# Kernel tuning notes

Measured on AMD Instinct MI355X. Metric: run time of the kernel, lower is better.

The kernel has to match this reference:

```python
import jax, jax.numpy as jnp
import numpy as np

N = 100000      # nodes
E = 1600000     # edges (before self-loops)
F_IN = 16       # num_node_features
HID = 16        # hid
HEADS = 4       # in_head == out_head
B = 64          # num graphs
G = 16          # num_global_features
NEG_SLOPE = 0.2


def gat_conv(x, src, dst, W, a_src, a_dst, b, concat):
    """PyG-style GATConv. x:[N,F], W:[F,H*C], a_src/a_dst:[H,C], b:[H*C] or [C]."""
    n = x.shape[0]
    H, C = a_src.shape
    h = (x @ W).reshape(n, H, C)                       # [N,H,C]
    alpha_s = (h * a_src).sum(-1)                      # [N,H]
    alpha_d = (h * a_dst).sum(-1)                      # [N,H]
    e = jax.nn.leaky_relu(alpha_s[src] + alpha_d[dst], NEG_SLOPE)  # [E',H]
    # segment softmax over destination nodes (stable; max is grad-free)
    m = jax.lax.stop_gradient(jax.ops.segment_max(e, dst, num_segments=n))
    ex = jnp.exp(e - m[dst])
    denom = jax.ops.segment_sum(ex, dst, num_segments=n)
    alpha = ex / (denom[dst] + 1e-16)                  # [E',H]
    out = jax.ops.segment_sum(h[src] * alpha[:, :, None], dst, num_segments=n)  # [N,H,C]
    out = out.reshape(n, H * C) if concat else out.mean(axis=1)
    return out + b


def setup_inputs() -> dict:
    key = jax.random.key(0)
    ks = jax.random.split(key, 24)
    s = 0.1
    inp = {
        "x": jax.random.normal(ks[0], (N, F_IN), jnp.float32),
        "stats": jax.random.normal(ks[1], (B, G), jnp.float32),
        # conv1: F_IN -> HID, heads=HEADS, concat=True
        "W1": jax.random.normal(ks[2], (F_IN, HEADS * HID), jnp.float32) * s,
        "a1s": jax.random.normal(ks[3], (HEADS, HID), jnp.float32) * s,
        "a1d": jax.random.normal(ks[4], (HEADS, HID), jnp.float32) * s,
        "b1": jnp.zeros((HEADS * HID,), jnp.float32),
        # conv2: HID*HEADS -> HID, heads=HEADS, concat=False
        "W2": jax.random.normal(ks[5], (HEADS * HID, HEADS * HID), jnp.float32) * s,
        "a2s": jax.random.normal(ks[6], (HEADS, HID), jnp.float32) * s,
        "a2d": jax.random.normal(ks[7], (HEADS, HID), jnp.float32) * s,
        "b2": jnp.zeros((HID,), jnp.float32),
        # conv3: HID -> HID, heads=HEADS, concat=False
        "W3": jax.random.normal(ks[8], (HID, HEADS * HID), jnp.float32) * s,
        "a3s": jax.random.normal(ks[9], (HEADS, HID), jnp.float32) * s,
        "a3d": jax.random.normal(ks[10], (HEADS, HID), jnp.float32) * s,
        "b3": jnp.zeros((HID,), jnp.float32),
        # MLP head
        "fw1": jax.random.normal(ks[11], (HID + G, 32), jnp.float32) * s,
        "fb1": jnp.zeros((32,), jnp.float32),
        "fw2": jax.random.normal(ks[12], (32, 16), jnp.float32) * s,
        "fb2": jnp.zeros((16,), jnp.float32),
        "fw3": jax.random.normal(ks[13], (16, 1), jnp.float32) * s,
        "fb3": jnp.zeros((1,), jnp.float32),
        "edge_index": jax.random.randint(ks[14], (2, E), 0, N, jnp.int64),
        "batch": jnp.sort(jax.random.randint(ks[15], (N,), 0, B, jnp.int64)),
    }
    return inp


def reference(x, stats, W1, a1s, a1d, b1, W2, a2s, a2d, b2, W3, a3s, a3d, b3,
              fw1, fb1, fw2, fb2, fw3, fb3, edge_index, batch):
    n = x.shape[0]
    loops = jnp.arange(n, dtype=edge_index.dtype)
    src = jnp.concatenate([edge_index[0], loops])  # add_self_loops=True (PyG default)
    dst = jnp.concatenate([edge_index[1], loops])
    h = jax.nn.elu(gat_conv(x, src, dst, W1, a1s, a1d, b1, True))
    h = jax.nn.elu(gat_conv(h, src, dst, W2, a2s, a2d, b2, False))
    h = gat_conv(h, src, dst, W3, a3s, a3d, b3, False)
    nb = stats.shape[0]
    pooled = jax.ops.segment_sum(h, batch, num_segments=nb)
    counts = jax.ops.segment_sum(jnp.ones((n,), h.dtype), batch, num_segments=nb)
    pooled = pooled / jnp.maximum(counts, 1.0)[:, None]   # global_mean_pool
    z = jnp.concatenate([pooled, stats], axis=1)
    z = jax.nn.relu(z @ fw1 + fb1)
    z = jax.nn.relu(z @ fw2 + fb2)
    return z @ fw3 + fb3
```

## Files before the change

### kernel.cpp

```cpp
#include <hip/hip_runtime.h>
#include <hip/hip_bf16.h>
#include <hip/hip_fp16.h>

#define NNODES 100000
#define NEDGES 1600000
#define NB     64
#define NG     16
#define POOL_SLOTS (NB * NG + NB)

#define BKT_SHIFT 7
#define NPB 128
#define NBKT ((NNODES + NPB - 1) / NPB)
#define BCAP 4096
#define SCAT_BLOCKS 256
#define NL1_BLOCKS 2048

typedef float vf2 __attribute__((ext_vector_type(2)));

__device__ __forceinline__ float leaky02(float v) {
    return v > 0.0f ? v : 0.2f * v;
}
__device__ __forceinline__ float elu1(float v) {
    return v > 0.0f ? v : __expf(v) - 1.0f;
}
__device__ __forceinline__ float dot4(float4 a, float4 b) {
    return a.x * b.x + a.y * b.y + a.z * b.z + a.w * b.w;
}

__device__ __forceinline__ int packQ4(float4 v) {
    int pk = __builtin_amdgcn_cvt_pk_fp8_f32(v.x, v.y, 0, false);
    pk = __builtin_amdgcn_cvt_pk_fp8_f32(v.z, v.w, pk, true);
    return pk;
}
__device__ __forceinline__ float4 loadQ4(const unsigned char* p) {
    int u = *(const int*)p;
    vf2 lo = __builtin_amdgcn_cvt_pk_f32_fp8(u, false);
    vf2 hi = __builtin_amdgcn_cvt_pk_f32_fp8(u, true);
    return make_float4(lo.x, lo.y, hi.x, hi.y);
}

__global__ void fold_prep(const float* __restrict__ W1,
                          const float* __restrict__ a1s,
                          const float* __restrict__ a1d,
                          const float* __restrict__ W3,
                          const float* __restrict__ a3s,
                          const float* __restrict__ a3d,
                          float* __restrict__ FOLD) {
    int t = threadIdx.x;
    int blk = t >> 6, h = (t >> 4) & 3, j = t & 15;
    const float* W = (blk < 2) ? W1 : W3;
    const float* a = (blk == 0) ? a1s : (blk == 1) ? a1d : (blk == 2) ? a3s : a3d;
    float s = 0.f;
    for (int c = 0; c < 16; ++c) s += W[j * 64 + h * 16 + c] * a[h * 16 + c];
    FOLD[t] = s;
}

__device__ __forceinline__ void nl1_body(const float* __restrict__ X,
                                         const float* __restrict__ FOLD,
                                         unsigned char* __restrict__ Xq,
                                         float* __restrict__ AS,
                                         float* __restrict__ AD, int n,
                                         int quad0, int nquads, int q) {
    float4 ws[4], wd[4];
#pragma unroll
    for (int h = 0; h < 4; ++h) {
        ws[h] = *(const float4*)&FOLD[h * 16 + 4 * q];
        wd[h] = *(const float4*)&FOLD[64 + h * 16 + 4 * q];
    }
    for (int i = quad0; i < n; i += nquads) {
        float4 x4 = *(const float4*)(X + (size_t)i * 16 + 4 * q);
        *(int*)(Xq + (size_t)i * 16 + 4 * q) = packQ4(x4);
        float s[4], d[4];
#pragma unroll
        for (int h = 0; h < 4; ++h) { s[h] = dot4(x4, ws[h]); d[h] = dot4(x4, wd[h]); }
#pragma unroll
        for (int h = 0; h < 4; ++h) {
            s[h] += __shfl_xor(s[h], 1); s[h] += __shfl_xor(s[h], 2);
            d[h] += __shfl_xor(d[h], 1); d[h] += __shfl_xor(d[h], 2);
        }
        if (q == 0) *(float4*)(AS + (size_t)i * 4) = make_float4(s[0], s[1], s[2], s[3]);
        if (q == 1) *(float4*)(AD + (size_t)i * 4) = make_float4(d[0], d[1], d[2], d[3]);
    }
}

__global__ void scatter_nl1(const int* __restrict__ src,
                            const int* __restrict__ dst,
                            int* __restrict__ bucketCnt,
                            unsigned int* __restrict__ pairs, int ne,
                            const float* __restrict__ X,
                            const float* __restrict__ FOLD,
                            unsigned char* __restrict__ Xq,
                            float* __restrict__ AS,
                            float* __restrict__ AD, int n) {
    __shared__ int hist[NBKT];
    __shared__ int base[NBKT];
    int tid = threadIdx.x;

    if (blockIdx.x >= SCAT_BLOCKS) {
        int q = tid & 3;
        int quad0 = ((blockIdx.x - SCAT_BLOCKS) * 256 + tid) >> 2;
        int nquads = (NL1_BLOCKS * 256) >> 2;
        nl1_body(X, FOLD, Xq, AS, AD, n, quad0, nquads, q);
        return;
    }

    for (int i = tid; i < NBKT; i += 256) hist[i] = 0;
    __syncthreads();

    int chunk = (ne + SCAT_BLOCKS - 1) / SCAT_BLOCKS;
    int beg = blockIdx.x * chunk;
    int end = min(beg + chunk, ne);

    for (int e0 = beg; e0 < end; e0 += 1024) {
        int d[4];
#pragma unroll
        for (int q = 0; q < 4; ++q) {
            int e = e0 + q * 256 + tid;
            d[q] = (e < end) ? dst[e] : -1;
        }
#pragma unroll
        for (int q = 0; q < 4; ++q)
            if (d[q] >= 0) atomicAdd(&hist[d[q] >> BKT_SHIFT], 1);
    }
    __syncthreads();

    for (int i = tid; i < NBKT; i += 256) {
        int h = hist[i];
        base[i] = h ? atomicAdd(&bucketCnt[i], h) : 0;
        hist[i] = 0;
    }
    __syncthreads();

    for (int e0 = beg; e0 < end; e0 += 1024) {
        int d[4], s[4];
#pragma unroll
        for (int q = 0; q < 4; ++q) {
            int e = e0 + q * 256 + tid;
            d[q] = (e < end) ? dst[e] : -1;
            s[q] = (e < end) ? src[e] : 0;
        }
        int r[4], bkt[4];
#pragma unroll
        for (int q = 0; q < 4; ++q) {
            if (d[q] >= 0) {
                bkt[q] = d[q] >> BKT_SHIFT;
                r[q] = base[bkt[q]] + atomicAdd(&hist[bkt[q]], 1);
            }
        }
#pragma unroll
        for (int q = 0; q < 4; ++q) {
            if (d[q] >= 0 && r[q] < BCAP)
                pairs[(size_t)bkt[q] * BCAP + r[q]] =
                    (unsigned)s[q] | ((unsigned)(d[q] & (NPB - 1)) << 20);
        }
    }
}

__global__ void bucket_sort(const unsigned int* __restrict__ pairs,
                            const int* __restrict__ bucketCnt,
                            int* __restrict__ srcs,
                            int* __restrict__ indptr, int n) {
    __shared__ int hist[NPB];
    __shared__ int offl[NPB];
    __shared__ int cur[NPB];
    __shared__ int red[256];
    __shared__ int lsrc[BCAP];
    int bkt = blockIdx.x;
    int t = threadIdx.x;
    int cnt = min(bucketCnt[bkt], BCAP);

    int partial = 0;
    for (int j = t; j < bkt; j += 256) partial += min(bucketCnt[j], BCAP);
    red[t] = partial;
    if (t < NPB) hist[t] = 0;
    __syncthreads();
    for (int s = 128; s > 0; s >>= 1) {
        if (t < s) red[t] += red[t + s];
        __syncthreads();
    }
    int boff = red[0];
    if (bkt == NBKT - 1 && t == 0) indptr[n] = boff + cnt;

    const unsigned int* __restrict__ p = pairs + (size_t)bkt * BCAP;
    unsigned int v[BCAP / 256];
#pragma unroll
    for (int i = 0; i < BCAP / 256; ++i) {
        int e = i * 256 + t;
        v[i] = 0u;
        if (e < cnt) {
            v[i] = p[e];
            atomicAdd(&hist[v[i] >> 20], 1);
        }
    }
    __syncthreads();
    if (t < NPB) offl[t] = hist[t];
    __syncthreads();
    for (int off = 1; off < NPB; off <<= 1) {
        int x = 0;
        if (t < NPB && t >= off) x = offl[t - off];
        __syncthreads();
        if (t < NPB && t >= off) offl[t] += x;
        __syncthreads();
    }
    if (t < NPB) {
        int ex = offl[t] - hist[t];
        cur[t] = ex;
        int node = bkt * NPB + t;
        if (node < n) indptr[node] = boff + ex;
    }
    __syncthreads();
#pragma unroll
    for (int i = 0; i < BCAP / 256; ++i) {
        int e = i * 256 + t;
        if (e < cnt) {
            int r = atomicAdd(&cur[v[i] >> 20], 1);
            lsrc[r] = (int)(v[i] & 0xFFFFFu);
        }
    }
    __syncthreads();
    for (int e = t; e < cnt; e += 256) srcs[boff + e] = lsrc[e];
}

__device__ __forceinline__ float4 gat_agg16(
    const unsigned char* __restrict__ Xq, const float* __restrict__ AS,
    const float* __restrict__ AD,
    const int* __restrict__ indptr, const int* __restrict__ srcs,
    int d, int grp, int sl, int head, int dq, float& denOut) {
    float ad  = AD[(size_t)d * 4 + head];
    float asd = AS[(size_t)d * 4 + head];
    float t0 = asd + ad;
    float wself = __expf(leaky02(t0));
    float den = wself;
    float4 x4s = loadQ4(Xq + (size_t)d * 16 + dq * 4);
    float4 acc = make_float4(wself * x4s.x, wself * x4s.y,
                             wself * x4s.z, wself * x4s.w);

    int beg = indptr[d], end = indptr[d + 1];
    for (int e0 = beg; e0 < end; e0 += 16) {
        int cnt = min(16, end - e0);
        int myS = (sl < cnt) ? srcs[e0 + sl] : 0;
        int j = 0;
        for (; j + 4 <= cnt; j += 4) {
            int s[4]; float a[4]; float4 h4[4];
#pragma unroll
            for (int q = 0; q < 4; ++q)
                s[q] = __shfl(myS, (grp << 4) + j + q);
#pragma unroll
            for (int q = 0; q < 4; ++q)
                a[q] = AS[(size_t)s[q] * 4 + head];
#pragma unroll
            for (int q = 0; q < 4; ++q)
                h4[q] = loadQ4(Xq + (size_t)s[q] * 16 + dq * 4);
#pragma unroll
            for (int q = 0; q < 4; ++q) {
                float t = a[q] + ad;
                float w = __expf(leaky02(t));
                den += w;
                acc.x += w * h4[q].x; acc.y += w * h4[q].y;
                acc.z += w * h4[q].z; acc.w += w * h4[q].w;
            }
        }
        for (; j < cnt; ++j) {
            int s = __shfl(myS, (grp << 4) + j);
            float t = AS[(size_t)s * 4 + head] + ad;
            float w = __expf(leaky02(t));
            float4 h4 = loadQ4(Xq + (size_t)s * 16 + dq * 4);
            den += w;
            acc.x += w * h4.x; acc.y += w * h4.y;
            acc.z += w * h4.z; acc.w += w * h4.w;
        }
    }
    denOut = den;
    return acc;
}

__device__ __forceinline__ float4 gat_agg64(
    const unsigned char* __restrict__ H, const float* __restrict__ AS,
    const float* __restrict__ AD,
    const int* __restrict__ indptr, const int* __restrict__ srcs,
    int d, int grp, int sl, int head, float& denOut) {
    float ad  = AD[(size_t)d * 4 + head];
    float asd = AS[(size_t)d * 4 + head];
    float t0 = asd + ad;
    float wself = __expf(leaky02(t0));
    float den = wself;
    float4 h4s = loadQ4(H + (size_t)d * 64 + sl * 4);
    float4 acc = make_float4(wself * h4s.x, wself * h4s.y,
                             wself * h4s.z, wself * h4s.w);

    int beg = indptr[d], end = indptr[d + 1];
    for (int e0 = beg; e0 < end; e0 += 16) {
        int cnt = min(16, end - e0);
        int myS = (sl < cnt) ? srcs[e0 + sl] : 0;
        int j = 0;
        for (; j + 4 <= cnt; j += 4) {
            int s[4]; float a[4]; float4 h4[4];
#pragma unroll
            for (int q = 0; q < 4; ++q)
                s[q] = __shfl(myS, (grp << 4) + j + q);
#pragma unroll
            for (int q = 0; q < 4; ++q)
                a[q] = AS[(size_t)s[q] * 4 + head];
#pragma unroll
            for (int q = 0; q < 4; ++q)
                h4[q] = loadQ4(H + (size_t)s[q] * 64 + sl * 4);
#pragma unroll
            for (int q = 0; q < 4; ++q) {
                float t = a[q] + ad;
                float w = __expf(leaky02(t));
                den += w;
                acc.x += w * h4[q].x; acc.y += w * h4[q].y;
                acc.z += w * h4[q].z; acc.w += w * h4[q].w;
            }
        }
        for (; j < cnt; ++j) {
            int s = __shfl(myS, (grp << 4) + j);
            float t = AS[(size_t)s * 4 + head] + ad;
            float w = __expf(leaky02(t));
            float4 h4 = loadQ4(H + (size_t)s * 64 + sl * 4);
            den += w;
            acc.x += w * h4.x; acc.y += w * h4.y;
            acc.z += w * h4.z; acc.w += w * h4.w;
        }
    }
    denOut = den;
    return acc;
}

__global__ void gat_pull_l1(const unsigned char* __restrict__ Xq,
                            const float* __restrict__ AS,
                            float* __restrict__ AD,
                            const int* __restrict__ indptr,
                            const int* __restrict__ srcs,
                            const float* __restrict__ W1,
                            const float* __restrict__ b1,
                            const float* __restrict__ W2,
                            const float* __restrict__ a2s,
                            const float* __restrict__ a2d,
                            unsigned char* __restrict__ Hq2,
                            float* __restrict__ AS2, int n) {
    __shared__ float w1s[16 * 64];
    __shared__ float w2s[64 * 64];
    for (int i = threadIdx.x; i < 16 * 64; i += 256) w1s[i] = W1[i];
    for (int i = threadIdx.x; i < 64 * 64; i += 256) w2s[i] = W2[i];
    __syncthreads();

    int lane = threadIdx.x & 63;
    int grp = lane >> 4, sl = lane & 15, head = sl >> 2, dq = sl & 3;
    int wave = (blockIdx.x * blockDim.x + threadIdx.x) >> 6;
    int nwaves = (gridDim.x * blockDim.x) >> 6;

    for (int d0 = wave * 4; d0 < n; d0 += nwaves * 4) {
        int d = d0 + grp;
        if (d >= n) continue;
        float den;
        float4 acc = gat_agg16(Xq, AS, AD, indptr, srcs, d, grp, sl, head, dq, den);
        float inv = 1.0f / (den + 1e-16f);
        float4 v = make_float4(acc.x * inv, acc.y * inv, acc.z * inv, acc.w * inv);

        float4 o = make_float4(0.f, 0.f, 0.f, 0.f);
#pragma unroll
        for (int p = 0; p < 4; ++p) {
            int srcl = (grp << 4) + head * 4 + p;
            float4 xq;
            xq.x = __shfl(v.x, srcl); xq.y = __shfl(v.y, srcl);
            xq.z = __shfl(v.z, srcl); xq.w = __shfl(v.w, srcl);
            const float* wr = &w1s[(4 * p) * 64 + 4 * sl];
            float4 w0 = *(const float4*)(wr);
            float4 w1r = *(const float4*)(wr + 64);
            float4 w2r = *(const float4*)(wr + 128);
            float4 w3r = *(const float4*)(wr + 192);
            o.x += xq.x * w0.x + xq.y * w1r.x + xq.z * w2r.x + xq.w * w3r.x;
            o.y += xq.x * w0.y + xq.y * w1r.y + xq.z * w2r.y + xq.w * w3r.y;
            o.z += xq.x * w0.z + xq.y * w1r.z + xq.z * w2r.z + xq.w * w3r.z;
            o.w += xq.x * w0.w + xq.y * w1r.w + xq.z * w2r.w + xq.w * w3r.w;
        }
        float4 bb = *(const float4*)(b1 + 4 * sl);
        o.x = elu1(o.x + bb.x); o.y = elu1(o.y + bb.y);
        o.z = elu1(o.z + bb.z); o.w = elu1(o.w + bb.w);

        float4 h2 = make_float4(0.f, 0.f, 0.f, 0.f);
#pragma unroll 4
        for (int p = 0; p < 16; ++p) {
            int srcl = (grp << 4) + p;
            float c0 = __shfl(o.x, srcl), c1v = __shfl(o.y, srcl);
            float c2v = __shfl(o.z, srcl), c3v = __shfl(o.w, srcl);
            const float* wr = &w2s[(4 * p) * 64 + 4 * sl];
            float4 w0 = *(const float4*)(wr);
            float4 w1r = *(const float4*)(wr + 64);
            float4 w2r = *(const float4*)(wr + 128);
            float4 w3r = *(const float4*)(wr + 192);
            h2.x += c0 * w0.x + c1v * w1r.x + c2v * w2r.x + c3v * w3r.x;
            h2.y += c0 * w0.y + c1v * w1r.y + c2v * w2r.y + c3v * w3r.y;
            h2.z += c0 * w0.z + c1v * w1r.z + c2v * w2r.z + c3v * w3r.z;
            h2.w += c0 * w0.w + c1v * w1r.w + c2v * w2r.w + c3v * w3r.w;
        }
        *(int*)(Hq2 + (size_t)d * 64 + 4 * sl) = packQ4(h2);

        float4 as4 = *(const float4*)(a2s + head * 16 + 4 * dq);
        float4 ad4 = *(const float4*)(a2d + head * 16 + 4 * dq);
        float s1 = dot4(h2, as4), s2 = dot4(h2, ad4);
        s1 += __shfl_xor(s1, 1); s1 += __shfl_xor(s1, 2);
        s2 += __shfl_xor(s2, 1); s2 += __shfl_xor(s2, 2);
        if (dq == 0) {
            AS2[(size_t)d * 4 + head] = s1;
            AD[(size_t)d * 4 + head] = s2;
        }
    }
}

__global__ void gat_pull_l2(const unsigned char* __restrict__ H,
                            const float* __restrict__ AS,
                            float* __restrict__ AD,
                            const int* __restrict__ indptr,
                            const int* __restrict__ srcs,
                            const float* __restrict__ bias,
                            const float* __restrict__ FOLD,
                            unsigned char* __restrict__ Xq3,
                            float* __restrict__ AS3, int n) {
    int lane = threadIdx.x & 63;
    int grp = lane >> 4, sl = lane & 15, head = sl >> 2, dq = sl & 3;
    int wave = (blockIdx.x * blockDim.x + threadIdx.x) >> 6;
    int nwaves = (gridDim.x * blockDim.x) >> 6;

    float4 w3s4 = *(const float4*)&FOLD[128 + head * 16 + 4 * dq];
    float4 w3d4 = *(const float4*)&FOLD[192 + head * 16 + 4 * dq];
    float4 b4 = *(const float4*)(bias + dq * 4);

    for (int d0 = wave * 4; d0 < n; d0 += nwaves * 4) {
        int d = d0 + grp;
        if (d >= n) continue;
        float den;
        float4 acc = gat_agg64(H, AS, AD, indptr, srcs, d, grp, sl, head, den);
        float inv = 1.0f / (den + 1e-16f);
        float4 v = make_float4(acc.x * inv, acc.y * inv, acc.z * inv, acc.w * inv);
#pragma unroll
        for (int off = 4; off <= 8; off <<= 1) {
            v.x += __shfl_xor(v.x, off);
            v.y += __shfl_xor(v.y, off);
            v.z += __shfl_xor(v.z, off);
            v.w += __shfl_xor(v.w, off);
        }
        v.x = elu1(0.25f * v.x + b4.x);
        v.y = elu1(0.25f * v.y + b4.y);
        v.z = elu1(0.25f * v.z + b4.z);
        v.w = elu1(0.25f * v.w + b4.w);
        if (sl < 4)
            *(int*)(Xq3 + (size_t)d * 16 + 4 * sl) = packQ4(v);
        float s1 = dot4(v, w3s4);
        float s2 = dot4(v, w3d4);
        s1 += __shfl_xor(s1, 1); s1 += __shfl_xor(s1, 2);
        s2 += __shfl_xor(s2, 1); s2 += __shfl_xor(s2, 2);
        if (dq == 0) {
            AS3[(size_t)d * 4 + head] = s1;
            AD[(size_t)d * 4 + head] = s2;
        }
    }
}

__global__ void gat_pull_l3(const unsigned char* __restrict__ Xq,
                            const float* __restrict__ AS,
                            const float* __restrict__ AD,
                            const int* __restrict__ indptr,
                            const int* __restrict__ srcs,
                            const float* __restrict__ W3,
                            const float* __restrict__ bias,
                            const int* __restrict__ batch,
                            float* __restrict__ PC, int n) {
    __shared__ float w3lds[16 * 64];
    __shared__ float lp[POOL_SLOTS];
    for (int i = threadIdx.x; i < 16 * 64; i += 256) w3lds[i] = W3[i];
    for (int i = threadIdx.x; i < POOL_SLOTS; i += 256) lp[i] = 0.f;
    __syncthreads();

    int lane = threadIdx.x & 63;
    int grp = lane >> 4, sl = lane & 15, head = sl >> 2, dq = sl & 3;
    int wave = (blockIdx.x * blockDim.x + threadIdx.x) >> 6;
    int nwaves = (gridDim.x * blockDim.x) >> 6;
    float4 b4 = *(const float4*)(bias + dq * 4);

    for (int d0 = wave * 4; d0 < n; d0 += nwaves * 4) {
        int d = d0 + grp;
        if (d < n) {
            float den;
            float4 acc = gat_agg16(Xq, AS, AD, indptr, srcs, d, grp, sl, head, dq, den);
            float inv = 1.0f / (den + 1e-16f);
            float4 v = make_float4(acc.x * inv, acc.y * inv, acc.z * inv, acc.w * inv);
            float4 o = make_float4(0.f, 0.f, 0.f, 0.f);
#pragma unroll
            for (int p = 0; p < 4; ++p) {
                int srcl = (grp << 4) + head * 4 + p;
                float4 xq;
                xq.x = __shfl(v.x, srcl); xq.y = __shfl(v.y, srcl);
                xq.z = __shfl(v.z, srcl); xq.w = __shfl(v.w, srcl);
                const float* wr = &w3lds[(4 * p) * 64 + head * 16 + 4 * dq];
                float4 w0 = *(const float4*)(wr);
                float4 w1r = *(const float4*)(wr + 64);
                float4 w2r = *(const float4*)(wr + 128);
                float4 w3r = *(const float4*)(wr + 192);
                o.x += xq.x * w0.x + xq.y * w1r.x + xq.z * w2r.x + xq.w * w3r.x;
                o.y += xq.x * w0.y + xq.y * w1r.y + xq.z * w2r.y + xq.w * w3r.y;
                o.z += xq.x * w0.z + xq.y * w1r.z + xq.z * w2r.z + xq.w * w3r.z;
                o.w += xq.x * w0.w + xq.y * w1r.w + xq.z * w2r.w + xq.w * w3r.w;
            }
#pragma unroll
            for (int off = 4; off <= 8; off <<= 1) {
                o.x += __shfl_xor(o.x, off);
                o.y += __shfl_xor(o.y, off);
                o.z += __shfl_xor(o.z, off);
                o.w += __shfl_xor(o.w, off);
            }
            o.x = 0.25f * o.x + b4.x; o.y = 0.25f * o.y + b4.y;
            o.z = 0.25f * o.z + b4.z; o.w = 0.25f * o.w + b4.w;
            if (sl < 4) {
                int b = batch[d];
                atomicAdd(&lp[b * 16 + sl * 4 + 0], o.x);
                atomicAdd(&lp[b * 16 + sl * 4 + 1], o.y);
                atomicAdd(&lp[b * 16 + sl * 4 + 2], o.z);
                atomicAdd(&lp[b * 16 + sl * 4 + 3], o.w);
                if (sl == 0) atomicAdd(&lp[NB * NG + b], 1.0f);
            }
        }
    }
    __syncthreads();
    for (int i = threadIdx.x; i < POOL_SLOTS; i += 256) {
        float s = lp[i];
        if (s != 0.f) atomicAdd(&PC[i], s);
    }
}

__global__ void mlp_head(const float* __restrict__ pooled_counts,
                         const float* __restrict__ stats,
                         const float* __restrict__ fw1, const float* __restrict__ fb1,
                         const float* __restrict__ fw2, const float* __restrict__ fb2,
                         const float* __restrict__ fw3, const float* __restrict__ fb3,
                         float* __restrict__ out) {
    int g = threadIdx.x;
    if (g >= NB) return;
    const float* pooled = pooled_counts;
    const float* counts = pooled_counts + NB * NG;
    float z[32];
    float inv = 1.0f / fmaxf(counts[g], 1.0f);
#pragma unroll
    for (int c = 0; c < 16; ++c) z[c] = pooled[g * 16 + c] * inv;
#pragma unroll
    for (int c = 0; c < 16; ++c) z[16 + c] = stats[g * 16 + c];

    float z1[32];
#pragma unroll
    for (int j = 0; j < 32; ++j) {
        float acc = fb1[j];
        for (int k = 0; k < 32; ++k) acc += z[k] * fw1[k * 32 + j];
        z1[j] = fmaxf(acc, 0.0f);
    }
    float z2[16];
#pragma unroll
    for (int j = 0; j < 16; ++j) {
        float acc = fb2[j];
        for (int k = 0; k < 32; ++k) acc += z1[k] * fw2[k * 16 + j];
        z2[j] = fmaxf(acc, 0.0f);
    }
    float acc = fb3[0];
#pragma unroll
    for (int k = 0; k < 16; ++k) acc += z2[k] * fw3[k];
    out[g] = acc;
}

extern "C" void kernel_launch(void* const* d_in, const int* in_sizes, int n_in,
                              void* d_out, int out_size, void* d_ws, size_t ws_size,
                              hipStream_t stream) {
    const float* x    = (const float*)d_in[0];
    const float* stats= (const float*)d_in[1];
    const float* W1   = (const float*)d_in[2];
    const float* a1s  = (const float*)d_in[3];
    const float* a1d  = (const float*)d_in[4];
    const float* b1   = (const float*)d_in[5];
    const float* W2   = (const float*)d_in[6];
    const float* a2s  = (const float*)d_in[7];
    const float* a2d  = (const float*)d_in[8];
    const float* b2   = (const float*)d_in[9];
    const float* W3   = (const float*)d_in[10];
    const float* a3s  = (const float*)d_in[11];
    const float* a3d  = (const float*)d_in[12];
    const float* b3   = (const float*)d_in[13];
    const float* fw1  = (const float*)d_in[14];
    const float* fb1  = (const float*)d_in[15];
    const float* fw2  = (const float*)d_in[16];
    const float* fb2  = (const float*)d_in[17];
    const float* fw3  = (const float*)d_in[18];
    const float* fb3  = (const float*)d_in[19];
    const int* ei     = (const int*)d_in[20];
    const int* batch  = (const int*)d_in[21];

    const int n = NNODES, ne = NEDGES;
    const int* srcI = ei;
    const int* dstI = ei + ne;

    unsigned char* Xq = (unsigned char*)d_ws;
    unsigned char* Hq2 = Xq + (size_t)n * 16;
    float* ASa  = (float*)(Hq2 + (size_t)n * 64);
    float* ASb  = ASa + (size_t)n * 4;
    float* AD   = ASb + (size_t)n * 4;
    float* FOLD = AD + (size_t)n * 4;
    float* PC   = FOLD + 256;
    int* bucketCnt = (int*)(PC + POOL_SLOTS);
    int* indptr    = bucketCnt + NBKT;
    int* srcs      = indptr + (n + 1);
    size_t off = (size_t)((char*)(srcs + ne) - (char*)d_ws);
    off = (off + 255) & ~(size_t)255;
    unsigned int* pairs = (unsigned int*)((char*)d_ws + off);

    const int TB = 256;
    const int pullBlocks = (n + 15) / 16;

    hipMemsetAsync(PC, 0, (POOL_SLOTS + NBKT) * sizeof(int), stream);

    fold_prep<<<1, 256, 0, stream>>>(W1, a1s, a1d, W3, a3s, a3d, FOLD);

    scatter_nl1<<<SCAT_BLOCKS + NL1_BLOCKS, TB, 0, stream>>>(
        srcI, dstI, bucketCnt, pairs, ne, x, FOLD, Xq, ASa, AD, n);
    bucket_sort<<<NBKT, TB, 0, stream>>>(pairs, bucketCnt, srcs, indptr, n);

    gat_pull_l1<<<pullBlocks, TB, 0, stream>>>(Xq, ASa, AD, indptr, srcs,
                                               W1, b1, W2, a2s, a2d,
                                               Hq2, ASb, n);

    gat_pull_l2<<<pullBlocks, TB, 0, stream>>>(Hq2, ASb, AD, indptr, srcs, b2,
                                               FOLD, Xq, ASa, n);

    gat_pull_l3<<<pullBlocks, TB, 0, stream>>>(Xq, ASa, AD, indptr, srcs,
                                               W3, b3, batch, PC, n);

    mlp_head<<<1, 64, 0, stream>>>(PC, stats, fw1, fb1, fw2, fb2, fw3, fb3,
                                   (float*)d_out);
}
```

Measured before the change: 318.1 us.

## Remap GAT pull kernels to four lanes per node with 16-feature rows

Restructures all three aggregation kernels so each destination node is handled by 4 lanes (one per head) instead of 16. Each lane loads a full 16-byte fp8 row with one uint4 load and keeps 16 accumulators, and edges are processed 4 at a time. The dense transforms become per-lane register matvecs, with fewer cross-lane shuffles, and small parameters are staged in LDS. The goal is to cut shuffle overhead and issue wider gathers per edge, at the cost of more registers per thread and less load balancing within a wave when node degrees vary.

After: 377.5 us. 1.19x slower.

```diff
diff --git a/kernel.cpp b/kernel.cpp
--- a/kernel.cpp
+++ b/kernel.cpp
@@ -32,11 +32,24 @@
     pk = __builtin_amdgcn_cvt_pk_fp8_f32(v.z, v.w, pk, true);
     return pk;
 }
-__device__ __forceinline__ float4 loadQ4(const unsigned char* p) {
-    int u = *(const int*)p;
-    vf2 lo = __builtin_amdgcn_cvt_pk_f32_fp8(u, false);
-    vf2 hi = __builtin_amdgcn_cvt_pk_f32_fp8(u, true);
-    return make_float4(lo.x, lo.y, hi.x, hi.y);
+__device__ __forceinline__ void fma16(uint4 u, float w, float* acc) {
+    unsigned uu[4] = {u.x, u.y, u.z, u.w};
+#pragma unroll
+    for (int b = 0; b < 4; ++b) {
+        vf2 lo = __builtin_amdgcn_cvt_pk_f32_fp8(uu[b], false);
+        vf2 hi = __builtin_amdgcn_cvt_pk_f32_fp8(uu[b], true);
+        acc[4 * b + 0] += w * lo.x;
+        acc[4 * b + 1] += w * lo.y;
+        acc[4 * b + 2] += w * hi.x;
+        acc[4 * b + 3] += w * hi.y;
+    }
+}
+__device__ __forceinline__ float4 pick4(const float* m, int h) {
+    float4 r = make_float4(m[0], m[1], m[2], m[3]);
+    if (h == 1) r = make_float4(m[4], m[5], m[6], m[7]);
+    if (h == 2) r = make_float4(m[8], m[9], m[10], m[11]);
+    if (h == 3) r = make_float4(m[12], m[13], m[14], m[15]);
+    return r;
 }
 
 __global__ void fold_prep(const float* __restrict__ W1,
@@ -221,110 +234,76 @@
     for (int e = t; e < cnt; e += 256) srcs[boff + e] = lsrc[e];
 }
 
-__device__ __forceinline__ float4 gat_agg16(
+__device__ __forceinline__ float agg16q(
     const unsigned char* __restrict__ Xq, const float* __restrict__ AS,
     const float* __restrict__ AD,
     const int* __restrict__ indptr, const int* __restrict__ srcs,
-    int d, int grp, int sl, int head, int dq, float& denOut) {
-    float ad  = AD[(size_t)d * 4 + head];
-    float asd = AS[(size_t)d * 4 + head];
-    float t0 = asd + ad;
-    float wself = __expf(leaky02(t0));
+    int d, int lane, int h, float* acc) {
+    float ad = AD[(size_t)d * 4 + h];
+    float wself = __expf(leaky02(AS[(size_t)d * 4 + h] + ad));
     float den = wself;
-    float4 x4s = loadQ4(Xq + (size_t)d * 16 + dq * 4);
-    float4 acc = make_float4(wself * x4s.x, wself * x4s.y,
-                             wself * x4s.z, wself * x4s.w);
+#pragma unroll
+    for (int k = 0; k < 16; ++k) acc[k] = 0.f;
+    uint4 xs = *(const uint4*)(Xq + (size_t)d * 16);
+    fma16(xs, wself, acc);
 
     int beg = indptr[d], end = indptr[d + 1];
-    for (int e0 = beg; e0 < end; e0 += 16) {
-        int cnt = min(16, end - e0);
-        int myS = (sl < cnt) ? srcs[e0 + sl] : 0;
-        int j = 0;
-        for (; j + 4 <= cnt; j += 4) {
-            int s[4]; float a[4]; float4 h4[4];
-#pragma unroll
-            for (int q = 0; q < 4; ++q)
-                s[q] = __shfl(myS, (grp << 4) + j + q);
-#pragma unroll
-            for (int q = 0; q < 4; ++q)
-                a[q] = AS[(size_t)s[q] * 4 + head];
-#pragma unroll
-            for (int q = 0; q < 4; ++q)
-                h4[q] = loadQ4(Xq + (size_t)s[q] * 16 + dq * 4);
-#pragma unroll
-            for (int q = 0; q < 4; ++q) {
-                float t = a[q] + ad;
-                float w = __expf(leaky02(t));
-                den += w;
-                acc.x += w * h4[q].x; acc.y += w * h4[q].y;
-                acc.z += w * h4[q].z; acc.w += w * h4[q].w;
-            }
-        }
-        for (; j < cnt; ++j) {
-            int s = __shfl(myS, (grp << 4) + j);
-            float t = AS[(size_t)s * 4 + head] + ad;
-            float w = __expf(leaky02(t));
-            float4 h4 = loadQ4(Xq + (size_t)s * 16 + dq * 4);
-            den += w;
-            acc.x += w * h4.x; acc.y += w * h4.y;
-            acc.z += w * h4.z; acc.w += w * h4.w;
-        }
-    }
-    denOut = den;
-    return acc;
-}
-
-__device__ __forceinline__ float4 gat_agg64(
+    int base = lane & ~3;
+    for (int e0 = beg; e0 < end; e0 += 4) {
+        int myS = srcs[min(e0 + h, end - 1)];
+        int s0 = __shfl(myS, base + 0), s1 = __shfl(myS, base + 1);
+        int s2 = __shfl(myS, base + 2), s3 = __shfl(myS, base + 3);
+        float a0 = AS[(size_t)s0 * 4 + h], a1 = AS[(size_t)s1 * 4 + h];
+        float a2 = AS[(size_t)s2 * 4 + h], a3 = AS[(size_t)s3 * 4 + h];
+        uint4 u0 = *(const uint4*)(Xq + (size_t)s0 * 16);
+        uint4 u1 = *(const uint4*)(Xq + (size_t)s1 * 16);
+        uint4 u2 = *(const uint4*)(Xq + (size_t)s2 * 16);
+        uint4 u3 = *(const uint4*)(Xq + (size_t)s3 * 16);
+        float w0 = (e0 + 0 < end) ? __expf(leaky02(a0 + ad)) : 0.f;
+        float w1 = (e0 + 1 < end) ? __expf(leaky02(a1 + ad)) : 0.f;
+        float w2 = (e0 + 2 < end) ? __expf(leaky02(a2 + ad)) : 0.f;
+        float w3 = (e0 + 3 < end) ? __expf(leaky02(a3 + ad)) : 0.f;
+        den += w0 + w1 + w2 + w3;
+        fma16(u0, w0, acc); fma16(u1, w1, acc);
+        fma16(u2, w2, acc); fma16(u3, w3, acc);
+    }
+    return den;
+}
+
+__device__ __forceinline__ float agg64q(
     const unsigned char* __restrict__ H, const float* __restrict__ AS,
     const float* __restrict__ AD,
     const int* __restrict__ indptr, const int* __restrict__ srcs,
-    int d, int grp, int sl, int head, float& denOut) {
-    float ad  = AD[(size_t)d * 4 + head];
-    float asd = AS[(size_t)d * 4 + head];
-    float t0 = asd + ad;
-    float wself = __expf(leaky02(t0));
+    int d, int lane, int h, float* acc) {
+    float ad = AD[(size_t)d * 4 + h];
+    float wself = __expf(leaky02(AS[(size_t)d * 4 + h] + ad));
     float den = wself;
-    float4 h4s = loadQ4(H + (size_t)d * 64 + sl * 4);
-    float4 acc = make_float4(wself * h4s.x, wself * h4s.y,
-                             wself * h4s.z, wself * h4s.w);
+#pragma unroll
+    for (int k = 0; k < 16; ++k) acc[k] = 0.f;
+    uint4 xs = *(const uint4*)(H + (size_t)d * 64 + h * 16);
+    fma16(xs, wself, acc);
 
     int beg = indptr[d], end = indptr[d + 1];
-    for (int e0 = beg; e0 < end; e0 += 16) {
-        int cnt = min(16, end - e0);
-        int myS = (sl < cnt) ? srcs[e0 + sl] : 0;
-        int j = 0;
-        for (; j + 4 <= cnt; j += 4) {
-            int s[4]; float a[4]; float4 h4[4];
-#pragma unroll
-            for (int q = 0; q < 4; ++q)
-                s[q] = __shfl(myS, (grp << 4) + j + q);
-#pragma unroll
-            for (int q = 0; q < 4; ++q)
-                a[q] = AS[(size_t)s[q] * 4 + head];
-#pragma unroll
-            for (int q = 0; q < 4; ++q)
-                h4[q] = loadQ4(H + (size_t)s[q] * 64 + sl * 4);
-#pragma unroll
-            for (int q = 0; q < 4; ++q) {
-                float t = a[q] + ad;
-                float w = __expf(leaky02(t));
-                den += w;
-                acc.x += w * h4[q].x; acc.y += w * h4[q].y;
-                acc.z += w * h4[q].z; acc.w += w * h4[q].w;
-            }
-        }
-        for (; j < cnt; ++j) {
-            int s = __shfl(myS, (grp << 4) + j);
-            float t = AS[(size_t)s * 4 + head] + ad;
-            float w = __expf(leaky02(t));
-            float4 h4 = loadQ4(H + (size_t)s * 64 + sl * 4);
-            den += w;
-            acc.x += w * h4.x; acc.y += w * h4.y;
-            acc.z += w * h4.z; acc.w += w * h4.w;
-        }
-    }
-    denOut = den;
-    return acc;
+    int base = lane & ~3;
+    for (int e0 = beg; e0 < end; e0 += 4) {
+        int myS = srcs[min(e0 + h, end - 1)];
+        int s0 = __shfl(myS, base + 0), s1 = __shfl(myS, base + 1);
+        int s2 = __shfl(myS, base + 2), s3 = __shfl(myS, base + 3);
+        float a0 = AS[(size_t)s0 * 4 + h], a1 = AS[(size_t)s1 * 4 + h];
+        float a2 = AS[(size_t)s2 * 4 + h], a3 = AS[(size_t)s3 * 4 + h];
+        uint4 u0 = *(const uint4*)(H + (size_t)s0 * 64 + h * 16);
+        uint4 u1 = *(const uint4*)(H + (size_t)s1 * 64 + h * 16);
+        uint4 u2 = *(const uint4*)(H + (size_t)s2 * 64 + h * 16);
+        uint4 u3 = *(const uint4*)(H + (size_t)s3 * 64 + h * 16);
+        float w0 = (e0 + 0 < end) ? __expf(leaky02(a0 + ad)) : 0.f;
+        float w1 = (e0 + 1 < end) ? __expf(leaky02(a1 + ad)) : 0.f;
+        float w2 = (e0 + 2 < end) ? __expf(leaky02(a2 + ad)) : 0.f;
+        float w3 = (e0 + 3 < end) ? __expf(leaky02(a3 + ad)) : 0.f;
+        den += w0 + w1 + w2 + w3;
+        fma16(u0, w0, acc); fma16(u1, w1, acc);
+        fma16(u2, w2, acc); fma16(u3, w3, acc);
+    }
+    return den;
 }
 
 __global__ void gat_pull_l1(const unsigned char* __restrict__ Xq,
@@ -341,71 +320,77 @@
                             float* __restrict__ AS2, int n) {
     __shared__ float w1s[16 * 64];
     __shared__ float w2s[64 * 64];
+    __shared__ float b1s[64], a2ss[64], a2ds[64];
     for (int i = threadIdx.x; i < 16 * 64; i += 256) w1s[i] = W1[i];
     for (int i = threadIdx.x; i < 64 * 64; i += 256) w2s[i] = W2[i];
-    __syncthreads();
-
-    int lane = threadIdx.x & 63;
-    int grp = lane >> 4, sl = lane & 15, head = sl >> 2, dq = sl & 3;
+    if (threadIdx.x < 64) {
+        b1s[threadIdx.x] = b1[threadIdx.x];
+        a2ss[threadIdx.x] = a2s[threadIdx.x];
+        a2ds[threadIdx.x] = a2d[threadIdx.x];
+    }
+    __syncthreads();
+
+    int lane = threadIdx.x & 63, h = lane & 3, g = lane >> 2;
     int wave = (blockIdx.x * blockDim.x + threadIdx.x) >> 6;
-    int nwaves = (gridDim.x * blockDim.x) >> 6;
-
-    for (int d0 = wave * 4; d0 < n; d0 += nwaves * 4) {
-        int d = d0 + grp;
+    int nw = (gridDim.x * blockDim.x) >> 6;
+    int base = lane & ~3;
+
+    for (int d0 = wave * 16; d0 < n; d0 += nw * 16) {
+        int d = d0 + g;
         if (d >= n) continue;
-        float den;
-        float4 acc = gat_agg16(Xq, AS, AD, indptr, srcs, d, grp, sl, head, dq, den);
+        float acc[16];
+        float den = agg16q(Xq, AS, AD, indptr, srcs, d, lane, h, acc);
         float inv = 1.0f / (den + 1e-16f);
-        float4 v = make_float4(acc.x * inv, acc.y * inv, acc.z * inv, acc.w * inv);
-
-        float4 o = make_float4(0.f, 0.f, 0.f, 0.f);
-#pragma unroll
-        for (int p = 0; p < 4; ++p) {
-            int srcl = (grp << 4) + head * 4 + p;
-            float4 xq;
-            xq.x = __shfl(v.x, srcl); xq.y = __shfl(v.y, srcl);
-            xq.z = __shfl(v.z, srcl); xq.w = __shfl(v.w, srcl);
-            const float* wr = &w1s[(4 * p) * 64 + 4 * sl];
-            float4 w0 = *(const float4*)(wr);
-            float4 w1r = *(const float4*)(wr + 64);
-            float4 w2r = *(const float4*)(wr + 128);
-            float4 w3r = *(const float4*)(wr + 192);
-            o.x += xq.x * w0.x + xq.y * w1r.x + xq.z * w2r.x + xq.w * w3r.x;
-            o.y += xq.x * w0.y + xq.y * w1r.y + xq.z * w2r.y + xq.w * w3r.y;
-            o.z += xq.x * w0.z + xq.y * w1r.z + xq.z * w2r.z + xq.w * w3r.z;
-            o.w += xq.x * w0.w + xq.y * w1r.w + xq.z * w2r.w + xq.w * w3r.w;
-        }
-        float4 bb = *(const float4*)(b1 + 4 * sl);
-        o.x = elu1(o.x + bb.x); o.y = elu1(o.y + bb.y);
-        o.z = elu1(o.z + bb.z); o.w = elu1(o.w + bb.w);
-
-        float4 h2 = make_float4(0.f, 0.f, 0.f, 0.f);
-#pragma unroll 4
-        for (int p = 0; p < 16; ++p) {
-            int srcl = (grp << 4) + p;
-            float c0 = __shfl(o.x, srcl), c1v = __shfl(o.y, srcl);
-            float c2v = __shfl(o.z, srcl), c3v = __shfl(o.w, srcl);
-            const float* wr = &w2s[(4 * p) * 64 + 4 * sl];
-            float4 w0 = *(const float4*)(wr);
-            float4 w1r = *(const float4*)(wr + 64);
-            float4 w2r = *(const float4*)(wr + 128);
-            float4 w3r = *(const float4*)(wr + 192);
-            h2.x += c0 * w0.x + c1v * w1r.x + c2v * w2r.x + c3v * w3r.x;
-            h2.y += c0 * w0.y + c1v * w1r.y + c2v * w2r.y + c3v * w3r.y;
-            h2.z += c0 * w0.z + c1v * w1r.z + c2v * w2r.z + c3v * w3r.z;
-            h2.w += c0 * w0.w + c1v * w1r.w + c2v * w2r.w + c3v * w3r.w;
-        }
-        *(int*)(Hq2 + (size_t)d * 64 + 4 * sl) = packQ4(h2);
-
-        float4 as4 = *(const float4*)(a2s + head * 16 + 4 * dq);
-        float4 ad4 = *(const float4*)(a2d + head * 16 + 4 * dq);
-        float s1 = dot4(h2, as4), s2 = dot4(h2, ad4);
-        s1 += __shfl_xor(s1, 1); s1 += __shfl_xor(s1, 2);
-        s2 += __shfl_xor(s2, 1); s2 += __shfl_xor(s2, 2);
-        if (dq == 0) {
-            AS2[(size_t)d * 4 + head] = s1;
-            AD[(size_t)d * 4 + head] = s2;
-        }
+
+        float c1[16];
+#pragma unroll
+        for (int j = 0; j < 16; ++j) c1[j] = b1s[h * 16 + j];
+#pragma unroll
+        for (int k = 0; k < 16; ++k) {
+            float vk = acc[k] * inv;
+            const float* wr = &w1s[k * 64 + h * 16];
+#pragma unroll
+            for (int jq = 0; jq < 4; ++jq) {
+                float4 w4 = *(const float4*)(wr + 4 * jq);
+                c1[4 * jq + 0] += vk * w4.x; c1[4 * jq + 1] += vk * w4.y;
+                c1[4 * jq + 2] += vk * w4.z; c1[4 * jq + 3] += vk * w4.w;
+            }
+        }
+#pragma unroll
+        for (int j = 0; j < 16; ++j) c1[j] = elu1(c1[j]);
+
+        float h2[16];
+#pragma unroll
+        for (int j = 0; j < 16; ++j) h2[j] = 0.f;
+#pragma unroll
+        for (int hh = 0; hh < 4; ++hh) {
+#pragma unroll
+            for (int kk = 0; kk < 16; ++kk) {
+                float c = __shfl(c1[kk], base + hh);
+                const float* wr = &w2s[(hh * 16 + kk) * 64 + h * 16];
+#pragma unroll
+                for (int jq = 0; jq < 4; ++jq) {
+                    float4 w4 = *(const float4*)(wr + 4 * jq);
+                    h2[4 * jq + 0] += c * w4.x; h2[4 * jq + 1] += c * w4.y;
+                    h2[4 * jq + 2] += c * w4.z; h2[4 * jq + 3] += c * w4.w;
+                }
+            }
+        }
+        uint4 pk;
+        pk.x = (unsigned)packQ4(make_float4(h2[0], h2[1], h2[2], h2[3]));
+        pk.y = (unsigned)packQ4(make_float4(h2[4], h2[5], h2[6], h2[7]));
+        pk.z = (unsigned)packQ4(make_float4(h2[8], h2[9], h2[10], h2[11]));
+        pk.w = (unsigned)packQ4(make_float4(h2[12], h2[13], h2[14], h2[15]));
+        *(uint4*)(Hq2 + (size_t)d * 64 + h * 16) = pk;
+
+        float s1 = 0.f, s2 = 0.f;
+#pragma unroll
+        for (int j = 0; j < 16; ++j) {
+            s1 += h2[j] * a2ss[h * 16 + j];
+            s2 += h2[j] * a2ds[h * 16 + j];
+        }
+        AS2[(size_t)d * 4 + h] = s1;
+        AD[(size_t)d * 4 + h] = s2;
     }
 }
 
@@ -414,47 +399,45 @@
                             float* __restrict__ AD,
                             const int* __restrict__ indptr,
                             const int* __restrict__ srcs,
-                            const float* __restrict__ bias,
+                            const float* __restrict__ b2,
                             const float* __restrict__ FOLD,
                             unsigned char* __restrict__ Xq3,
                             float* __restrict__ AS3, int n) {
-    int lane = threadIdx.x & 63;
-    int grp = lane >> 4, sl = lane & 15, head = sl >> 2, dq = sl & 3;
+    __shared__ float fold_lds[256];
+    __shared__ float b2s[16];
+    if (threadIdx.x < 256) fold_lds[threadIdx.x] = FOLD[threadIdx.x];
+    if (threadIdx.x < 16) b2s[threadIdx.x] = b2[threadIdx.x];
+    __syncthreads();
+
+    int lane = threadIdx.x & 63, h = lane & 3, g = lane >> 2;
     int wave = (blockIdx.x * blockDim.x + threadIdx.x) >> 6;
-    int nwaves = (gridDim.x * blockDim.x) >> 6;
-
-    float4 w3s4 = *(const float4*)&FOLD[128 + head * 16 + 4 * dq];
-    float4 w3d4 = *(const float4*)&FOLD[192 + head * 16 + 4 * dq];
-    float4 b4 = *(const float4*)(bias + dq * 4);
-
-    for (int d0 = wave * 4; d0 < n; d0 += nwaves * 4) {
-        int d = d0 + grp;
+    int nw = (gridDim.x * blockDim.x) >> 6;
+
+    for (int d0 = wave * 16; d0 < n; d0 += nw * 16) {
+        int d = d0 + g;
         if (d >= n) continue;
-        float den;
-        float4 acc = gat_agg64(H, AS, AD, indptr, srcs, d, grp, sl, head, den);
+        float acc[16];
+        float den = agg64q(H, AS, AD, indptr, srcs, d, lane, h, acc);
         float inv = 1.0f / (den + 1e-16f);
-        float4 v = make_float4(acc.x * inv, acc.y * inv, acc.z * inv, acc.w * inv);
-#pragma unroll
-        for (int off = 4; off <= 8; off <<= 1) {
-            v.x += __shfl_xor(v.x, off);
-            v.y += __shfl_xor(v.y, off);
-            v.z += __shfl_xor(v.z, off);
-            v.w += __shfl_xor(v.w, off);
-        }
-        v.x = elu1(0.25f * v.x + b4.x);
-        v.y = elu1(0.25f * v.y + b4.y);
-        v.z = elu1(0.25f * v.z + b4.z);
-        v.w = elu1(0.25f * v.w + b4.w);
-        if (sl < 4)
-            *(int*)(Xq3 + (size_t)d * 16 + 4 * sl) = packQ4(v);
-        float s1 = dot4(v, w3s4);
-        float s2 = dot4(v, w3d4);
-        s1 += __shfl_xor(s1, 1); s1 += __shfl_xor(s1, 2);
-        s2 += __shfl_xor(s2, 1); s2 += __shfl_xor(s2, 2);
-        if (dq == 0) {
-            AS3[(size_t)d * 4 + head] = s1;
-            AD[(size_t)d * 4 + head] = s2;
-        }
+        float m[16];
+#pragma unroll
+        for (int k = 0; k < 16; ++k) m[k] = acc[k] * inv;
+#pragma unroll
+        for (int k = 0; k < 16; ++k) {
+            m[k] += __shfl_xor(m[k], 1);
+            m[k] += __shfl_xor(m[k], 2);
+            m[k] = elu1(0.25f * m[k] + b2s[k]);
+        }
+        float4 mv = pick4(m, h);
+        *(int*)(Xq3 + (size_t)d * 16 + 4 * h) = packQ4(mv);
+        float s1 = 0.f, s2 = 0.f;
+#pragma unroll
+        for (int k = 0; k < 16; ++k) {
+            s1 += m[k] * fold_lds[128 + h * 16 + k];
+            s2 += m[k] * fold_lds[192 + h * 16 + k];
+        }
+        AS3[(size_t)d * 4 + h] = s1;
+        AD[(size_t)d * 4 + h] = s2;
     }
 }
 
@@ -464,62 +447,54 @@
                             const int* __restrict__ indptr,
                             const int* __restrict__ srcs,
                             const float* __restrict__ W3,
-                            const float* __restrict__ bias,
+                            const float* __restrict__ b3,
                             const int* __restrict__ batch,
                             float* __restrict__ PC, int n) {
-    __shared__ float w3lds[16 * 64];
+    __shared__ float w3s[16 * 64];
     __shared__ float lp[POOL_SLOTS];
-    for (int i = threadIdx.x; i < 16 * 64; i += 256) w3lds[i] = W3[i];
+    for (int i = threadIdx.x; i < 16 * 64; i += 256) w3s[i] = W3[i];
     for (int i = threadIdx.x; i < POOL_SLOTS; i += 256) lp[i] = 0.f;
     __syncthreads();
 
-    int lane = threadIdx.x & 63;
-    int grp = lane >> 4, sl = lane & 15, head = sl >> 2, dq = sl & 3;
+    int lane = threadIdx.x & 63, h = lane & 3, g = lane >> 2;
     int wave = (blockIdx.x * blockDim.x + threadIdx.x) >> 6;
-    int nwaves = (gridDim.x * blockDim.x) >> 6;
-    float4 b4 = *(const float4*)(bias + dq * 4);
-
-    for (int d0 = wave * 4; d0 < n; d0 += nwaves * 4) {
-        int d = d0 + grp;
+    int nw = (gridDim.x * blockDim.x) >> 6;
+
+    for (int d0 = wave * 16; d0 < n; d0 += nw * 16) {
+        int d = d0 + g;
         if (d < n) {
-            float den;
-            float4 acc = gat_agg16(Xq, AS, AD, indptr, srcs, d, grp, sl, head, dq, den);
+            float acc[16];
+            float den = agg16q(Xq, AS, AD, indptr, srcs, d, lane, h, acc);
             float inv = 1.0f / (den + 1e-16f);
-            float4 v = make_float4(acc.x * inv, acc.y * inv, acc.z * inv, acc.w * inv);
-            float4 o = make_float4(0.f, 0.f, 0.f, 0.f);
-#pragma unroll
-            for (int p = 0; p < 4; ++p) {
-                int srcl = (grp << 4) + head * 4 + p;
-                float4 xq;
-                xq.x = __shfl(v.x, srcl); xq.y = __shfl(v.y, srcl);
-                xq.z = __shfl(v.z, srcl); xq.w = __shfl(v.w, srcl);
-                const float* wr = &w3lds[(4 * p) * 64 + head * 16 + 4 * dq];
-                float4 w0 = *(const float4*)(wr);
-                float4 w1r = *(const float4*)(wr + 64);
-                float4 w2r = *(const float4*)(wr + 128);
-                float4 w3r = *(const float4*)(wr + 192);
-                o.x += xq.x * w0.x + xq.y * w1r.x + xq.z * w2r.x + xq.w * w3r.x;
-                o.y += xq.x * w0.y + xq.y * w1r.y + xq.z * w2r.y + xq.w * w3r.y;
-                o.z += xq.x * w0.z + xq.y * w1r.z + xq.z * w2r.z + xq.w * w3r.z;
-                o.w += xq.x * w0.w + xq.y * w1r.w + xq.z * w2r.w + xq.w * w3r.w;
+            float o[16];
+#pragma unroll
+            for (int j = 0; j < 16; ++j) o[j] = 0.f;
+#pragma unroll
+            for (int k = 0; k < 16; ++k) {
+                float vk = acc[k] * inv;
+                const float* wr = &w3s[k * 64 + h * 16];
+#pragma unroll
+                for (int jq = 0; jq < 4; ++jq) {
+                    float4 w4 = *(const float4*)(wr + 4 * jq);
+                    o[4 * jq + 0] += vk * w4.x; o[4 * jq + 1] += vk * w4.y;
+                    o[4 * jq + 2] += vk * w4.z; o[4 * jq + 3] += vk * w4.w;
+                }
             }
 #pragma unroll
-            for (int off = 4; off <= 8; off <<= 1) {
-                o.x += __shfl_xor(o.x, off);
-                o.y += __shfl_xor(o.y, off);
-                o.z += __shfl_xor(o.z, off);
-                o.w += __shfl_xor(o.w, off);
+            for (int j = 0; j < 16; ++j) {
+                o[j] += __shfl_xor(o[j], 1);
+                o[j] += __shfl_xor(o[j], 2);
             }
-            o.x = 0.25f * o.x + b4.x; o.y = 0.25f * o.y + b4.y;
-            o.z = 0.25f * o.z + b4.z; o.w = 0.25f * o.w + b4.w;
-            if (sl < 4) {
-                int b = batch[d];
-                atomicAdd(&lp[b * 16 + sl * 4 + 0], o.x);
-                atomicAdd(&lp[b * 16 + sl * 4 + 1], o.y);
-                atomicAdd(&lp[b * 16 + sl * 4 + 2], o.z);
-                atomicAdd(&lp[b * 16 + sl * 4 + 3], o.w);
-                if (sl == 0) atomicAdd(&lp[NB * NG + b], 1.0f);
-            }
+            float4 ov = pick4(o, h);
+            float4 bv = *(const float4*)(b3 + 4 * h);
+            ov.x = 0.25f * ov.x + bv.x; ov.y = 0.25f * ov.y + bv.y;
+            ov.z = 0.25f * ov.z + bv.z; ov.w = 0.25f * ov.w + bv.w;
+            int b = batch[d];
+            atomicAdd(&lp[b * 16 + 4 * h + 0], ov.x);
+            atomicAdd(&lp[b * 16 + 4 * h + 1], ov.y);
+            atomicAdd(&lp[b * 16 + 4 * h + 2], ov.z);
+            atomicAdd(&lp[b * 16 + 4 * h + 3], ov.w);
+            if (h == 0) atomicAdd(&lp[NB * NG + b], 1.0f);
         }
     }
     __syncthreads();
@@ -611,7 +586,7 @@
     unsigned int* pairs = (unsigned int*)((char*)d_ws + off);
 
     const int TB = 256;
-    const int pullBlocks = (n + 15) / 16;
+    const int pullBlocks = (n + 63) / 64;
 
     hipMemsetAsync(PC, 0, (POOL_SLOTS + NBKT) * sizeof(int), stream);
 
```

## Sort destination nodes by degree within chunks to balance pull-kernel waves

Applied to the files above, without the earlier changes.

Adds a deg_sort kernel that builds a permutation grouping nodes of similar in-degree within 4096-node chunks. The three GAT pull kernels then walk nodes through this permutation, so the four nodes sharing a wave have similar edge counts and lanes idle less in the 16-edge loop. The cost is an extra kernel launch, one more indirection per node, and less locality for the scattered per-node writes and for the pooling in layer 3. Degrees are Poisson around 16, so the imbalance it removes may be small.

Measured after the change: 356.4 us. +12.0%, slower.

```diff
diff --git a/kernel.cpp b/kernel.cpp
--- a/kernel.cpp
+++ b/kernel.cpp
@@ -14,6 +14,7 @@
 #define BCAP 4096
 #define SCAT_BLOCKS 256
 #define NL1_BLOCKS 2048
+#define DS_CHUNK 4096
 
 typedef float vf2 __attribute__((ext_vector_type(2)));
 
@@ -221,6 +222,32 @@
     for (int e = t; e < cnt; e += 256) srcs[boff + e] = lsrc[e];
 }
 
+__global__ void deg_sort(const int* __restrict__ indptr,
+                         int* __restrict__ perm, int n) {
+    __shared__ int hist[64];
+    __shared__ int cur[64];
+    int t = threadIdx.x;
+    int c0 = blockIdx.x * DS_CHUNK;
+    int c1 = min(c0 + DS_CHUNK, n);
+    if (t < 64) hist[t] = 0;
+    __syncthreads();
+    for (int i = c0 + t; i < c1; i += 256) {
+        int deg = min(indptr[i + 1] - indptr[i], 63);
+        atomicAdd(&hist[deg], 1);
+    }
+    __syncthreads();
+    if (t == 0) {
+        int acc = 0;
+        for (int k = 0; k < 64; ++k) { int h = hist[k]; cur[k] = acc; acc += h; }
+    }
+    __syncthreads();
+    for (int i = c0 + t; i < c1; i += 256) {
+        int deg = min(indptr[i + 1] - indptr[i], 63);
+        int pos = atomicAdd(&cur[deg], 1);
+        perm[c0 + pos] = i;
+    }
+}
+
 __device__ __forceinline__ float4 gat_agg16(
     const unsigned char* __restrict__ Xq, const float* __restrict__ AS,
     const float* __restrict__ AD,
@@ -332,6 +359,7 @@
                             float* __restrict__ AD,
                             const int* __restrict__ indptr,
                             const int* __restrict__ srcs,
+                            const int* __restrict__ perm,
                             const float* __restrict__ W1,
                             const float* __restrict__ b1,
                             const float* __restrict__ W2,
@@ -350,9 +378,10 @@
     int wave = (blockIdx.x * blockDim.x + threadIdx.x) >> 6;
     int nwaves = (gridDim.x * blockDim.x) >> 6;
 
-    for (int d0 = wave * 4; d0 < n; d0 += nwaves * 4) {
-        int d = d0 + grp;
-        if (d >= n) continue;
+    for (int i0 = wave * 4; i0 < n; i0 += nwaves * 4) {
+        int idx = i0 + grp;
+        if (idx >= n) continue;
+        int d = perm[idx];
         float den;
         float4 acc = gat_agg16(Xq, AS, AD, indptr, srcs, d, grp, sl, head, dq, den);
         float inv = 1.0f / (den + 1e-16f);
@@ -414,6 +443,7 @@
                             float* __restrict__ AD,
                             const int* __restrict__ indptr,
                             const int* __restrict__ srcs,
+                            const int* __restrict__ perm,
                             const float* __restrict__ bias,
                             const float* __restrict__ FOLD,
                             unsigned char* __restrict__ Xq3,
@@ -427,9 +457,10 @@
     float4 w3d4 = *(const float4*)&FOLD[192 + head * 16 + 4 * dq];
     float4 b4 = *(const float4*)(bias + dq * 4);
 
-    for (int d0 = wave * 4; d0 < n; d0 += nwaves * 4) {
-        int d = d0 + grp;
-        if (d >= n) continue;
+    for (int i0 = wave * 4; i0 < n; i0 += nwaves * 4) {
+        int idx = i0 + grp;
+        if (idx >= n) continue;
+        int d = perm[idx];
         float den;
         float4 acc = gat_agg64(H, AS, AD, indptr, srcs, d, grp, sl, head, den);
         float inv = 1.0f / (den + 1e-16f);
@@ -463,6 +494,7 @@
                             const float* __restrict__ AD,
                             const int* __restrict__ indptr,
                             const int* __restrict__ srcs,
+                            const int* __restrict__ perm,
                             const float* __restrict__ W3,
                             const float* __restrict__ bias,
                             const int* __restrict__ batch,
@@ -479,9 +511,10 @@
     int nwaves = (gridDim.x * blockDim.x) >> 6;
     float4 b4 = *(const float4*)(bias + dq * 4);
 
-    for (int d0 = wave * 4; d0 < n; d0 += nwaves * 4) {
-        int d = d0 + grp;
-        if (d < n) {
+    for (int i0 = wave * 4; i0 < n; i0 += nwaves * 4) {
+        int idx = i0 + grp;
+        if (idx < n) {
+            int d = perm[idx];
             float den;
             float4 acc = gat_agg16(Xq, AS, AD, indptr, srcs, d, grp, sl, head, dq, den);
             float inv = 1.0f / (den + 1e-16f);
@@ -606,12 +639,14 @@
     int* bucketCnt = (int*)(PC + POOL_SLOTS);
     int* indptr    = bucketCnt + NBKT;
     int* srcs      = indptr + (n + 1);
-    size_t off = (size_t)((char*)(srcs + ne) - (char*)d_ws);
+    int* perm      = srcs + ne;
+    size_t off = (size_t)((char*)(perm + n) - (char*)d_ws);
     off = (off + 255) & ~(size_t)255;
     unsigned int* pairs = (unsigned int*)((char*)d_ws + off);
 
     const int TB = 256;
     const int pullBlocks = (n + 15) / 16;
+    const int dsBlocks = (n + DS_CHUNK - 1) / DS_CHUNK;
 
     hipMemsetAsync(PC, 0, (POOL_SLOTS + NBKT) * sizeof(int), stream);
 
@@ -620,15 +655,16 @@
     scatter_nl1<<<SCAT_BLOCKS + NL1_BLOCKS, TB, 0, stream>>>(
         srcI, dstI, bucketCnt, pairs, ne, x, FOLD, Xq, ASa, AD, n);
     bucket_sort<<<NBKT, TB, 0, stream>>>(pairs, bucketCnt, srcs, indptr, n);
-
-    gat_pull_l1<<<pullBlocks, TB, 0, stream>>>(Xq, ASa, AD, indptr, srcs,
+    deg_sort<<<dsBlocks, TB, 0, stream>>>(indptr, perm, n);
+
+    gat_pull_l1<<<pullBlocks, TB, 0, stream>>>(Xq, ASa, AD, indptr, srcs, perm,
                                                W1, b1, W2, a2s, a2d,
                                                Hq2, ASb, n);
 
-    gat_pull_l2<<<pullBlocks, TB, 0, stream>>>(Hq2, ASb, AD, indptr, srcs, b2,
-                                               FOLD, Xq, ASa, n);
-
-    gat_pull_l3<<<pullBlocks, TB, 0, stream>>>(Xq, ASa, AD, indptr, srcs,
+    gat_pull_l2<<<pullBlocks, TB, 0, stream>>>(Hq2, ASb, AD, indptr, srcs, perm,
+                                               b2, FOLD, Xq, ASa, n);
+
+    gat_pull_l3<<<pullBlocks, TB, 0, stream>>>(Xq, ASa, AD, indptr, srcs, perm,
                                                W3, b3, batch, PC, n);
 
     mlp_head<<<1, 64, 0, stream>>>(PC, stats, fw1, fb1, fw2, fb2, fw3, fb3,
```
